# Performance work log

Hardware: AMD Instinct MI355X
Metric: run time of the kernel (lower is better)

## Reference

```python
import jax, jax.numpy as jnp
import numpy as np

MAXTIME = 1406073600
MINTIME = 832550400
SPAN = 10000
TIME_EMB = 100
N_GATE = 8
NUM_INTEREST = 4
DIM = 64
SEQ = 256
BATCH = 1024
ALPHA = 0.1
PI = 3.14159  # matches the literal in the source


def _build_time_table():
    # TimeEncoder: interleaved sin/cos positional table over time buckets.
    n = MAXTIME // SPAN + 3
    pos = np.arange(n, dtype=np.float64)[:, None]
    div = np.exp(np.arange(TIME_EMB // 2, dtype=np.float64) * -(np.log(10000.0) / TIME_EMB))[None, :]
    te = np.zeros((n, TIME_EMB), dtype=np.float32)
    te[:, 0::2] = np.sin(pos * div)
    te[:, 1::2] = np.cos(pos * div)
    return jnp.asarray(te)

_TIME_TABLE = _build_time_table()


def _time_encode(t):
    idx = (t / SPAN).astype(jnp.int32)
    return _TIME_TABLE[idx - jnp.min(idx)]


def setup_inputs() -> dict:
    key = jax.random.key(0)
    ks = jax.random.split(key, 11)
    B, S, D, NI, G = BATCH, SEQ, DIM, NUM_INTEREST, N_GATE
    item_his_emb = jax.random.normal(ks[0], (B, S, D), jnp.float32)
    item_eb = jax.random.normal(ks[1], (B, D), jnp.float32)
    # query times near maxtime, history times strictly earlier -> positive deltas
    t_batch = MAXTIME - 1e6 * jax.random.uniform(ks[2], (B,), jnp.float32)
    t_his = MINTIME + (MAXTIME - MINTIME - 1e6) * jax.random.uniform(ks[3], (B, S), jnp.float32)
    mask = (jax.random.uniform(ks[4], (B, S)) > 0.3).astype(jnp.float32)
    W1 = jax.random.normal(ks[5], (3 * TIME_EMB, 100), jnp.float32) / np.sqrt(3 * TIME_EMB)
    b1 = jnp.zeros((100,), jnp.float32)
    W2 = jax.random.normal(ks[6], (100, 1), jnp.float32) * 0.1
    b2 = jnp.zeros((1,), jnp.float32)
    phase = 100000.0 * jax.random.uniform(ks[7], (1, 1, G), jnp.float32)
    tao = 86400.0 * jnp.array([[[1, 2, 7, 14, 30, 60, 365, 730]]], jnp.float32)
    ratio = 0.3 * jax.random.uniform(ks[8], (1, 1, G), jnp.float32)
    gate_emb = jax.random.normal(ks[9], (1, D, G), jnp.float32)
    w_bilinear = jax.random.normal(ks[10], (S, NI * D, D), jnp.float32)
    return {"item_his_emb": item_his_emb, "item_eb": item_eb, "t_batch": t_batch,
            "t_his": t_his, "mask": mask, "W1": W1, "b1": b1, "W2": W2, "b2": b2,
            "phase": phase, "tao": tao, "ratio": ratio, "gate_emb": gate_emb,
            "w_bilinear": w_bilinear, "ta": 2}


def reference(item_his_emb, item_eb, t_batch, t_his, mask, W1, b1, W2, b2,
              phase, tao, ratio, gate_emb, w_bilinear, ta):
    B, S, D = item_his_emb.shape
    NI = NUM_INTEREST
    # --- time factor ---
    t_tiled = jnp.broadcast_to(t_batch[:, None], (B, S))
    time_feature = jnp.concatenate([_time_encode(t_tiled), _time_encode(t_his),
                                    _time_encode(t_tiled - t_his)], axis=2)  # [B,S,300]
    hidden1 = jax.nn.relu(time_feature @ W1 + b1)
    t_factor = jnp.transpose(jax.nn.sigmoid(hidden1 @ W2 + b2), (0, 2, 1))  # [B,1,S]
    # --- circadian gate factor ---
    phi = jnp.mod(t_his[:, :, None] - phase, tao) / tao  # [B,S,G]
    gate = jnp.where(phi < ratio, jnp.maximum(jnp.sin(PI * phi / ratio), 0.0), ALPHA * phi)
    gate_ratio = jax.nn.softmax(jnp.einsum('bsd,dg->bsg', item_his_emb, gate_emb[0]), axis=2) * gate
    g_factor = jnp.sum(gate_ratio, axis=2)[:, None, :]  # [B,1,S]
    reg1 = jnp.linalg.norm(t_factor)
    reg2 = jnp.linalg.norm(ratio) + jnp.linalg.norm(phase) / 100000.0
    # ta == 2 branch
    loss_reg = 0.1 * reg1 + 1.0 * reg2 + 1.0 / reg1 + 0.1 / reg2
    factor = jnp.broadcast_to(t_factor + g_factor, (B, NI, S))
    # --- bilinear_type == 2 projection ---
    item_emb_hat = jnp.einsum('skd,bsd->bsk', w_bilinear, item_his_emb)  # [B,S,NI*D]
    item_emb_hat = item_emb_hat.reshape(B, S, NI, D).transpose(0, 2, 1, 3)  # [B,NI,S,D]
    hat_iter = jax.lax.stop_gradient(item_emb_hat)
    # --- dynamic routing, 3 iterations ---
    cw = jnp.zeros((B, NI, S), item_his_emb.dtype)
    amask = mask[:, None, :]
    cap = None
    for i in range(3):
        sw = jax.nn.softmax(cw, axis=1)           # softmax over interests
        sw = jnp.where(amask == 0, 0.0, sw)
        src = hat_iter if i < 2 else item_emb_hat
        cap = jnp.einsum('bks,bksd->bkd', sw, src)  # [B,NI,D]
        n2 = jnp.sum(cap * cap, axis=-1, keepdims=True)
        cap = (n2 / (1.0 + n2) / jnp.sqrt(n2 + 1e-9)) * cap  # squash
        if i < 2:
            delta = jnp.einsum('bksd,bkd->bks', hat_iter, cap) * factor
            cw = cw + delta
    interest_capsule = cap  # [B,NI,D]
    # --- hard readout ---
    atten = jax.nn.softmax(jnp.einsum('bkd,bd->bk', interest_capsule, item_eb), axis=1)
    readout = interest_capsule[jnp.arange(B), jnp.argmax(atten, axis=1)]  # [B,D]
    return interest_capsule, readout, loss_reg
```

## Files before the change

kernel.cpp:

```cpp
#include <hip/hip_runtime.h>
#include <math.h>
#include <limits.h>

#define BB 1024
#define SS 256
#define DD 64
#define NI 4
#define NG 8
#define TE_N 100
#define PMAX 57420
#define PMAXP 57424
#define P0MAX 128
#define TPB2 64
#define NPAIR ((size_t)BB*SS)

typedef _Float16 half8 __attribute__((ext_vector_type(8)));
typedef _Float16 half4 __attribute__((ext_vector_type(4)));
typedef float f32x4 __attribute__((ext_vector_type(4)));

#define OFF_FTHT  ((size_t)0)
#define OFF_FDFT  ((size_t)TE_N*PMAXP)
#define OFF_GTBP  (OFF_FDFT + (size_t)TE_N*PMAXP)
#define OFF_FAC   (OFF_GTBP + (size_t)TE_N*P0MAX)
#define OFF_SCAL  (OFF_FAC + (size_t)BB*SS)
#define OFF_REC   (OFF_SCAL + 160)
#define OFF_SREC  (OFF_REC + NPAIR*2)
#define OFF_ZP    (OFF_SREC + NPAIR*2)
#define OFF_HAT   (OFF_ZP + 4*NPAIR)

__device__ inline float dpp_add_xor1(float x){
    int i = __builtin_bit_cast(int, x);
    int p = __builtin_amdgcn_update_dpp(i, i, 0xB1, 0xF, 0xF, true);
    return x + __builtin_bit_cast(float, p);
}
__device__ inline float dpp_add_xor2(float x){
    int i = __builtin_bit_cast(int, x);
    int p = __builtin_amdgcn_update_dpp(i, i, 0x4E, 0xF, 0xF, true);
    return x + __builtin_bit_cast(float, p);
}
__device__ inline float swz_add_xor16(float x){
    int i = __builtin_bit_cast(int, x);
    int p = __builtin_amdgcn_ds_swizzle(i, 0x401F);
    return x + __builtin_bit_cast(float, p);
}

__global__ void k_init(float* ws){
    int t = threadIdx.x;
    int* ib = (int*)(ws + OFF_SCAL);
    if (t == 0){
        ib[0] = INT_MAX; ib[1] = INT_MAX; ib[2] = INT_MAX;
        ws[OFF_SCAL + 4] = 0.0f;
    }
    if (t >= 8 && t < 136) ib[t] = 0;
}

__global__ void k_min(const float* __restrict__ tb, const float* __restrict__ th, float* ws){
    int gid = blockIdx.x * blockDim.x + threadIdx.x;
    int stride = gridDim.x * blockDim.x;
    int m0 = INT_MAX, m1 = INT_MAX, m2 = INT_MAX;
    for (int i = gid; i < BB*SS; i += stride){
        float t  = th[i];
        float t2 = tb[i >> 8];
        int i1 = (int)(t / 10000.0f);
        int i2 = (int)((t2 - t) / 10000.0f);
        m1 = min(m1, i1);
        m2 = min(m2, i2);
    }
    if (gid < BB) m0 = (int)(tb[gid] / 10000.0f);
    #pragma unroll
    for (int off = 1; off < 64; off <<= 1){
        m0 = min(m0, __shfl_xor(m0, off));
        m1 = min(m1, __shfl_xor(m1, off));
        m2 = min(m2, __shfl_xor(m2, off));
    }
    if ((threadIdx.x & 63) == 0){
        int* mi = (int*)(ws + OFF_SCAL);
        atomicMin(mi + 0, m0);
        atomicMin(mi + 1, m1);
        atomicMin(mi + 2, m2);
    }
}

__global__ void __launch_bounds__(256) k_tables(const float* __restrict__ W1, float* ws){
    int pbase = blockIdx.x * TPB2;
    int t = threadIdx.x;
    __shared__ float te[TPB2][102];
    for (int idx = t; idx < TPB2*50; idx += 256){
        int pp = idx / 50, h = idx - pp*50;
        double div = exp((double)h * -0.09210340371976184);
        double a = (double)(pbase + pp) * div;
        te[pp][2*h]   = (float)sin(a);
        te[pp][2*h+1] = (float)cos(a);
    }
    __syncthreads();
    #pragma unroll 5
    for (int k = 0; k < 25; k++){
        int o = t + 256*k;
        int j = __builtin_amdgcn_readfirstlane(o >> 6);
        int pp = o & 63;
        int p = pbase + pp;
        float a1 = 0.f, a2 = 0.f;
        for (int i = 0; i < TE_N; i++){
            float v = te[pp][i];
            a1 += v * W1[(100+i)*100 + j];
            a2 += v * W1[(200+i)*100 + j];
        }
        if (p < PMAX){
            ws[OFF_FTHT + (size_t)j*PMAXP + p] = a1;
            ws[OFF_FDFT + (size_t)j*PMAXP + p] = a2;
        }
    }
}

__global__ void k_gtbP(const float* __restrict__ W1, const float* __restrict__ b1, float* ws){
    int p0 = blockIdx.x;
    int t = threadIdx.x;
    __shared__ float te[TE_N];
    if (t < TE_N/2){
        double div = exp((double)t * -0.09210340371976184);
        double a = (double)p0 * div;
        te[2*t]   = (float)sin(a);
        te[2*t+1] = (float)cos(a);
    }
    __syncthreads();
    if (t < TE_N){
        float a1 = b1[t];
        for (int i = 0; i < TE_N; i++) a1 += te[i] * W1[i*100 + t];
        ws[OFF_GTBP + (size_t)t*P0MAX + p0] = a1;
    }
}

__global__ void __launch_bounds__(256) k_hist(const float* __restrict__ tb,
                                              const float* __restrict__ th, float* ws){
    __shared__ int lh[64];
    int t = threadIdx.x;
    if (t < 64) lh[t] = 0;
    __syncthreads();
    int gid = blockIdx.x*256 + t;
    int b = gid >> 8;
    const int* mi = (const int*)(ws + OFF_SCAL);
    float thv = th[gid], tbv = tb[b];
    int p1 = (int)(thv / 10000.0f) - mi[1];
    int p2 = (int)((tbv - thv) / 10000.0f) - mi[2];
    int p0 = (int)(tbv / 10000.0f) - mi[0];
    p1 = min(max(p1, 0), PMAX-1);
    p2 = min(max(p2, 0), PMAX-1);
    p0 = min(max(p0, 0), P0MAX-1);
    ((uint2*)(ws + OFF_REC))[gid] =
        make_uint2((unsigned)p1 | ((unsigned)p2 << 16), (unsigned)gid | ((unsigned)p0 << 20));
    atomicAdd(&lh[p1 >> 10], 1);
    __syncthreads();
    if (t < 64 && lh[t]) atomicAdd((int*)(ws + OFF_SCAL) + 8 + t, lh[t]);
}

__global__ void k_scan(float* ws){
    if (threadIdx.x == 0){
        int* g   = (int*)(ws + OFF_SCAL) + 8;
        int* cur = (int*)(ws + OFF_SCAL) + 72;
        int acc = 0;
        for (int i = 0; i < 64; i++){ cur[i] = acc; acc += g[i]; }
    }
}

__global__ void __launch_bounds__(256) k_scatter(float* ws){
    __shared__ int lh[64], lbase[64];
    int t = threadIdx.x;
    if (t < 64) lh[t] = 0;
    __syncthreads();
    int gid = blockIdx.x*256 + t;
    uint2 r = ((const uint2*)(ws + OFF_REC))[gid];
    int bkt = (int)(r.x & 0xFFFFu) >> 10;
    int myloc = atomicAdd(&lh[bkt], 1);
    __syncthreads();
    if (t < 64 && lh[t]) lbase[t] = atomicAdd((int*)(ws + OFF_SCAL) + 72 + t, lh[t]);
    __syncthreads();
    ((uint2*)(ws + OFF_SREC))[lbase[bkt] + myloc] = r;
}

__global__ void __launch_bounds__(256) k_factor2(const float* __restrict__ W2, float* ws){
    int t = threadIdx.x;
    int bid = blockIdx.x;
    int jh  = blockIdx.y;
    int sbid = (bid & 7)*128 + (bid >> 3);
    int q = sbid*256 + t;
    uint2 r = ((const uint2*)(ws + OFF_SREC))[q];
    int p1  = (int)(r.x & 0xFFFFu);
    int p2  = (int)(r.x >> 16);
    int p0  = (int)(r.y >> 20);

    const float* ft = ws + OFF_FTHT + (size_t)(jh*25)*PMAXP + p1;
    const float* fd = ws + OFF_FDFT + (size_t)(jh*25)*PMAXP + p2;
    const float* gp = ws + OFF_GTBP + (size_t)(jh*25)*P0MAX + p0;
    const float* w2 = W2 + jh*25;

    float z = 0.f;
    #pragma unroll
    for (int j = 0; j < 25; j++){
        float a = ft[(size_t)j*PMAXP];
        float c = fd[(size_t)j*PMAXP];
        float g = gp[(size_t)j*P0MAX];
        z += fmaxf(g + a + c, 0.f) * w2[j];
    }
    ws[OFF_ZP + (size_t)jh*NPAIR + q] = z;
}

__global__ void __launch_bounds__(256) k_fsig(const float* __restrict__ b2, float* ws){
    int q = blockIdx.x*256 + threadIdx.x;
    float z = (ws[OFF_ZP + q] + ws[OFF_ZP + NPAIR + q])
            + (ws[OFF_ZP + 2*NPAIR + q] + ws[OFF_ZP + 3*NPAIR + q]);
    unsigned ry = ((const uint2*)(ws + OFF_SREC))[q].y;
    int gid = (int)(ry & 0xFFFFFu);
    float tf = 1.f / (1.f + expf(-(z + b2[0])));
    ws[OFF_FAC + gid] = tf;
    float r1 = tf * tf;
    #pragma unroll
    for (int off = 1; off < 64; off <<= 1) r1 += __shfl_xor(r1, off);
    if ((threadIdx.x & 63) == 0) atomicAdd(ws + OFF_SCAL + 4, r1);
}

__global__ void __launch_bounds__(256) k_gate(const float* __restrict__ X,
      const float* __restrict__ th_, const float* __restrict__ phase,
      const float* __restrict__ tao, const float* __restrict__ ratio,
      const float* __restrict__ ge, float* ws){
    __shared__ float sge[NG][DD];
    int t = threadIdx.x;
    for (int i = t; i < DD*NG; i += 256) sge[i & 7][i >> 3] = ge[i];
    __syncthreads();
    int gid = blockIdx.x * 256 + t;

    float lg[NG];
    #pragma unroll
    for (int g = 0; g < NG; g++) lg[g] = 0.f;
    const float4* xr = (const float4*)(X + (size_t)gid*DD);
    #pragma unroll 4
    for (int dc = 0; dc < 16; dc++){
        float4 xv = xr[dc];
        #pragma unroll
        for (int g = 0; g < NG; g++){
            lg[g] += xv.x*sge[g][dc*4+0] + xv.y*sge[g][dc*4+1]
                   + xv.z*sge[g][dc*4+2] + xv.w*sge[g][dc*4+3];
        }
    }
    float mx = lg[0];
    #pragma unroll
    for (int g = 1; g < NG; g++) mx = fmaxf(mx, lg[g]);
    float thv = th_[gid];
    float es = 0.f, gf = 0.f;
    #pragma unroll
    for (int g = 0; g < NG; g++){
        float e = expf(lg[g] - mx);
        es += e;
        float phv = fmodf(thv - phase[g], tao[g]) / tao[g];
        float gv = (phv < ratio[g]) ? fmaxf(sinf(3.14159f*phv/ratio[g]), 0.f) : 0.1f*phv;
        gf += e * gv;
    }
    ws[OFF_FAC + gid] += gf / es;
}

__global__ void __launch_bounds__(512, 2)
k_hat(const float* __restrict__ X, const float* __restrict__ Wb,
      float* __restrict__ hat, int b0, int nb){
    int btile = blockIdx.x;
    int s     = blockIdx.y;
    int t     = threadIdx.x;
    int rows = nb - btile*64; if (rows > 64) rows = 64;

    __shared__ _Float16 lds[40960];

    const float* xbase = X + ((size_t)(b0 + btile*64)*SS + s)*DD;
    #pragma unroll
    for (int i = 0; i < 2; i++){
        int q = t + 512*i;
        int r = q >> 4, jf = q & 15;
        float4 v;
        if (r < rows) v = *(const float4*)(xbase + (size_t)r*SS*DD + jf*4);
        else { v.x = 0.f; v.y = 0.f; v.z = 0.f; v.w = 0.f; }
        half4 h, l;
        h.x = (_Float16)v.x; h.y = (_Float16)v.y; h.z = (_Float16)v.z; h.w = (_Float16)v.w;
        l.x = (_Float16)(v.x - (float)h.x); l.y = (_Float16)(v.y - (float)h.y);
        l.z = (_Float16)(v.z - (float)h.z); l.w = (_Float16)(v.w - (float)h.w);
        int bt = r >> 4, rowin = r & 15;
        int j0 = jf*4;
        int kk = j0 >> 5, jb = (j0 & 31) >> 3, e0 = j0 & 7;
        int lane = rowin + 16*jb;
        int base = ((bt*2 + kk)*2)*512 + lane*8 + e0;
        *(half4*)(lds + base)       = h;
        *(half4*)(lds + base + 512) = l;
    }
    const float* wbase = Wb + (size_t)s*16384;
    #pragma unroll
    for (int i = 0; i < 8; i++){
        int q = t + 512*i;
        int kd = q >> 4, jf = q & 15;
        float4 v = *(const float4*)(wbase + kd*64 + jf*4);
        half4 h, l;
        h.x = (_Float16)v.x; h.y = (_Float16)v.y; h.z = (_Float16)v.z; h.w = (_Float16)v.w;
        l.x = (_Float16)(v.x - (float)h.x); l.y = (_Float16)(v.y - (float)h.y);
        l.z = (_Float16)(v.z - (float)h.z); l.w = (_Float16)(v.w - (float)h.w);
        int kdt = kd >> 4, rowin = kd & 15;
        int j0 = jf*4;
        int kk = j0 >> 5, jb = (j0 & 31) >> 3, e0 = j0 & 7;
        int lane = rowin + 16*jb;
        int base = 8192 + ((kdt*2 + kk)*2)*512 + lane*8 + e0;
        *(half4*)(lds + base)       = h;
        *(half4*)(lds + base + 512) = l;
    }
    __syncthreads();

    int w    = t >> 6;
    int lane = t & 63;
    int wbt  = w >> 1;
    int kdh  = w & 1;

    half8 a[2][2];
    #pragma unroll
    for (int kk = 0; kk < 2; kk++)
        #pragma unroll
        for (int hl = 0; hl < 2; hl++)
            a[kk][hl] = *(half8*)(lds + ((wbt*2 + kk)*2 + hl)*512 + lane*8);

    int brow = (lane >> 4) * 4;
    int bcol = lane & 15;

    #pragma unroll
    for (int kdti = 0; kdti < 8; kdti++){
        int kdt = kdh*8 + kdti;
        const _Float16* wb0 = lds + 8192 + ((kdt*2 + 0)*2)*512 + lane*8;
        const _Float16* wb1 = lds + 8192 + ((kdt*2 + 1)*2)*512 + lane*8;
        half8 bh0 = *(half8*)(wb0);
        half8 bl0 = *(half8*)(wb0 + 512);
        half8 bh1 = *(half8*)(wb1);
        half8 bl1 = *(half8*)(wb1 + 512);
        f32x4 acc = {0.f, 0.f, 0.f, 0.f};
        acc = __builtin_amdgcn_mfma_f32_16x16x32_f16(a[0][0], bh0, acc, 0, 0, 0);
        acc = __builtin_amdgcn_mfma_f32_16x16x32_f16(a[0][0], bl0, acc, 0, 0, 0);
        acc = __builtin_amdgcn_mfma_f32_16x16x32_f16(a[0][1], bh0, acc, 0, 0, 0);
        acc = __builtin_amdgcn_mfma_f32_16x16x32_f16(a[1][0], bh1, acc, 0, 0, 0);
        acc = __builtin_amdgcn_mfma_f32_16x16x32_f16(a[1][0], bl1, acc, 0, 0, 0);
        acc = __builtin_amdgcn_mfma_f32_16x16x32_f16(a[1][1], bh1, acc, 0, 0, 0);
        int kd = kdt*16 + bcol;
        #pragma unroll
        for (int r = 0; r < 4; r++){
            int rl = wbt*16 + brow + r;
            if (rl < rows)
                hat[((size_t)(btile*64 + rl)*SS + s)*256 + kd] = acc[r];
        }
    }
}

__global__ void __launch_bounds__(1024) k_route(const float* __restrict__ eb,
                                                const float* __restrict__ mask_,
                                                const float* __restrict__ ws,
                                                const float* __restrict__ hat,
                                                float* __restrict__ out, int b0){
    int bl = blockIdx.x;
    int b = b0 + bl;
    int t = threadIdx.x;
    int lane = t & 63, wv = t >> 6;
    int k = (lane >> 2) & 3;
    int s_local = (lane & 3) | (((lane >> 4) & 3) << 2);
    int s = wv * 16 + s_local;
    __shared__ float part[16][4][64];
    __shared__ float capl[4][68];
    __shared__ float logits[4];
    __shared__ int kms;

    float hat_r[64];
    const float4* hsrc = (const float4*)(hat + (size_t)bl*65536 + ((size_t)s*4 + k)*64);
    #pragma unroll
    for (int jc = 0; jc < 16; jc++){
        float4 v = hsrc[jc];
        hat_r[4*jc] = v.x; hat_r[4*jc+1] = v.y; hat_r[4*jc+2] = v.z; hat_r[4*jc+3] = v.w;
    }
    float fac = ws[OFF_FAC + (size_t)b*SS + s];
    float mk = mask_[(size_t)b*SS + s];
    float cw = 0.f;
    float capv = 0.f;

    for (int it = 0; it < 3; ++it){
        float sw;
        if (it == 0){
            sw = (mk == 0.f) ? 0.f : 0.25f;
        } else {
            float m = fmaxf(cw, __shfl_xor(cw, 4)); m = fmaxf(m, __shfl_xor(m, 8));
            float e = expf(cw - m);
            float ssum = e + __shfl_xor(e, 4); ssum += __shfl_xor(ssum, 8);
            sw = (mk == 0.f) ? 0.f : (e / ssum);
        }

        #pragma unroll
        for (int c = 0; c < 4; c++){
            float tmp[16];
            #pragma unroll
            for (int i = 0; i < 16; i++) tmp[i] = sw * hat_r[c*16 + i];
            #pragma unroll
            for (int i = 0; i < 16; i++) tmp[i] = dpp_add_xor1(tmp[i]);
            #pragma unroll
            for (int i = 0; i < 16; i++) tmp[i] = dpp_add_xor2(tmp[i]);
            #pragma unroll
            for (int i = 0; i < 16; i++) tmp[i] = swz_add_xor16(tmp[i]);
            #pragma unroll
            for (int i = 0; i < 16; i++) tmp[i] += __shfl_xor(tmp[i], 32);
            if ((lane & 0x33) == 0){
                float* dst = &part[wv][lane >> 2][c*16];
                #pragma unroll
                for (int i = 0; i < 4; i++)
                    ((float4*)dst)[i] = make_float4(tmp[4*i], tmp[4*i+1], tmp[4*i+2], tmp[4*i+3]);
            }
        }
        __syncthreads();
        if (t < 256){
            int k2 = t >> 6, d = t & 63;
            float cp = 0.f;
            #pragma unroll
            for (int w2 = 0; w2 < 16; w2++) cp += part[w2][k2][d];
            float q = cp * cp;
            #pragma unroll
            for (int msk = 1; msk < 64; msk <<= 1) q += __shfl_xor(q, msk);
            float sc = q / ((1.f + q) * sqrtf(q + 1e-9f));
            capv = sc * cp;
            capl[k2][d] = capv;
        }
        __syncthreads();
        if (it < 2){
            const float4* cp4 = (const float4*)&capl[k][0];
            float dot = 0.f;
            #pragma unroll
            for (int jc = 0; jc < 16; jc++){
                float4 v = cp4[jc];
                dot += hat_r[4*jc]*v.x + hat_r[4*jc+1]*v.y + hat_r[4*jc+2]*v.z + hat_r[4*jc+3]*v.w;
            }
            cw += dot * fac;
        }
        __syncthreads();
    }

    if (t < 256){
        int k2 = t >> 6, d = t & 63;
        out[(size_t)b*256 + t] = capv;
        float qq = capv * eb[(size_t)b*DD + d];
        #pragma unroll
        for (int msk = 1; msk < 64; msk <<= 1) qq += __shfl_xor(qq, msk);
        if (lane == 0) logits[k2] = qq;
    }
    __syncthreads();
    if (t == 0){
        float best = logits[0]; int km = 0;
        for (int kk = 1; kk < 4; kk++) if (logits[kk] > best){ best = logits[kk]; km = kk; }
        kms = km;
    }
    __syncthreads();
    if (t < 64) out[(size_t)BB*256 + (size_t)b*64 + t] = capl[kms][t];
}

__global__ void k_final(const float* __restrict__ phase, const float* __restrict__ ratio,
                        float* ws, float* __restrict__ out){
    if (threadIdx.x == 0){
        float r2a = 0.f, r2b = 0.f;
        for (int g = 0; g < NG; g++){ r2a += ratio[g]*ratio[g]; r2b += phase[g]*phase[g]; }
        float reg2 = sqrtf(r2a) + sqrtf(r2b) / 100000.0f;
        float reg1 = sqrtf(ws[OFF_SCAL + 4]);
        out[(size_t)BB*256 + (size_t)BB*64] = 0.1f*reg1 + reg2 + 1.0f/reg1 + 0.1f/reg2;
    }
}

extern "C" void kernel_launch(void* const* d_in, const int* in_sizes, int n_in,
                              void* d_out, int out_size, void* d_ws, size_t ws_size,
                              hipStream_t stream){
    const float* Xh = (const float*)d_in[0];
    const float* eb = (const float*)d_in[1];
    const float* tb = (const float*)d_in[2];
    const float* th = (const float*)d_in[3];
    const float* mk = (const float*)d_in[4];
    const float* W1 = (const float*)d_in[5];
    const float* b1 = (const float*)d_in[6];
    const float* W2 = (const float*)d_in[7];
    const float* b2 = (const float*)d_in[8];
    const float* ph = (const float*)d_in[9];
    const float* ta = (const float*)d_in[10];
    const float* ra = (const float*)d_in[11];
    const float* ge = (const float*)d_in[12];
    const float* wb = (const float*)d_in[13];
    float* out = (float*)d_out;
    float* ws  = (float*)d_ws;

    hipLaunchKernelGGL(k_init,    dim3(1),     dim3(256), 0, stream, ws);
    hipLaunchKernelGGL(k_min,     dim3(256),   dim3(256), 0, stream, tb, th, ws);
    hipLaunchKernelGGL(k_tables,  dim3((PMAX+TPB2-1)/TPB2), dim3(256), 0, stream, W1, ws);
    hipLaunchKernelGGL(k_gtbP,    dim3(P0MAX), dim3(128), 0, stream, W1, b1, ws);
    hipLaunchKernelGGL(k_hist,    dim3(BB),    dim3(256), 0, stream, tb, th, ws);
    hipLaunchKernelGGL(k_scan,    dim3(1),     dim3(64),  0, stream, ws);
    hipLaunchKernelGGL(k_scatter, dim3(BB),    dim3(256), 0, stream, ws);
    hipLaunchKernelGGL(k_factor2, dim3(1024, 4), dim3(256), 0, stream, W2, ws);
    hipLaunchKernelGGL(k_fsig,    dim3(1024),  dim3(256), 0, stream, b2, ws);
    hipLaunchKernelGGL(k_gate,    dim3(BB),    dim3(256), 0, stream, Xh, th, ph, ta, ra, ge, ws);

    long wfloats  = (long)(ws_size / sizeof(float));
    long hatavail = wfloats - (long)OFF_HAT;
    int CH = (int)(hatavail / 65536);
    if (CH > BB) CH = BB;
    if (CH >= 128) CH &= ~127;
    if (CH < 1)  CH = 1;
    float* hatbuf = ws + OFF_HAT;
    for (int c0 = 0; c0 < BB; c0 += CH){
        int nb = BB - c0; if (nb > CH) nb = CH;
        int nbt = (nb + 63) / 64;
        hipLaunchKernelGGL(k_hat,   dim3(nbt, 256), dim3(512),  0, stream, Xh, wb, hatbuf, c0, nb);
        hipLaunchKernelGGL(k_route, dim3(nb),       dim3(1024), 0, stream, eb, mk, ws, hatbuf, out, c0);
    }
    hipLaunchKernelGGL(k_final, dim3(1), dim3(64), 0, stream, ph, ra, ws, out);
}
```

Baseline: 608.7 us.

## Register-tile time-table projection per output column and stage results through LDS

The table-building kernel now gives each thread one output column and has it accumulate over 16 table positions in registers. Each W1 weight is therefore loaded once per 16 positions instead of once per position. Results are transposed through shared memory so the global stores stay coalesced along the position axis. The cost is more blocks with smaller 128-thread groups, 28 of the 128 threads idle during the compute phase, and higher register use.

```diff
diff --git a/kernel.cpp b/kernel.cpp
--- a/kernel.cpp
+++ b/kernel.cpp
@@ -11,7 +11,7 @@
 #define PMAX 57420
 #define PMAXP 57424
 #define P0MAX 128
-#define TPB2 64
+#define TPB 16
 #define NPAIR ((size_t)BB*SS)
 
 typedef _Float16 half8 __attribute__((ext_vector_type(8)));
@@ -81,11 +81,13 @@
     }
 }
 
-__global__ void __launch_bounds__(256) k_tables(const float* __restrict__ W1, float* ws){
-    int pbase = blockIdx.x * TPB2;
-    int t = threadIdx.x;
-    __shared__ float te[TPB2][102];
-    for (int idx = t; idx < TPB2*50; idx += 256){
+__global__ void __launch_bounds__(128) k_tables(const float* __restrict__ W1, float* ws){
+    int pbase = blockIdx.x * TPB;
+    int t = threadIdx.x;
+    __shared__ float te[TPB][TE_N];
+    __shared__ float tr1[TPB][104];
+    __shared__ float tr2[TPB][104];
+    for (int idx = t; idx < TPB*50; idx += 128){
         int pp = idx / 50, h = idx - pp*50;
         double div = exp((double)h * -0.09210340371976184);
         double a = (double)(pbase + pp) * div;
@@ -93,21 +95,33 @@
         te[pp][2*h+1] = (float)cos(a);
     }
     __syncthreads();
-    #pragma unroll 5
-    for (int k = 0; k < 25; k++){
-        int o = t + 256*k;
-        int j = __builtin_amdgcn_readfirstlane(o >> 6);
-        int pp = o & 63;
+    if (t < TE_N){
+        float a1[TPB], a2[TPB];
+        #pragma unroll
+        for (int pp = 0; pp < TPB; pp++){ a1[pp] = 0.f; a2[pp] = 0.f; }
+        for (int i = 0; i < TE_N; i++){
+            float w1v = W1[(100+i)*100 + t];
+            float w2v = W1[(200+i)*100 + t];
+            #pragma unroll
+            for (int pp = 0; pp < TPB; pp++){
+                float v = te[pp][i];
+                a1[pp] += v * w1v;
+                a2[pp] += v * w2v;
+            }
+        }
+        #pragma unroll
+        for (int pp = 0; pp < TPB; pp++){
+            tr1[pp][t] = a1[pp];
+            tr2[pp][t] = a2[pp];
+        }
+    }
+    __syncthreads();
+    for (int idx = t; idx < TPB*TE_N; idx += 128){
+        int j = idx >> 4, pp = idx & 15;
         int p = pbase + pp;
-        float a1 = 0.f, a2 = 0.f;
-        for (int i = 0; i < TE_N; i++){
-            float v = te[pp][i];
-            a1 += v * W1[(100+i)*100 + j];
-            a2 += v * W1[(200+i)*100 + j];
-        }
         if (p < PMAX){
-            ws[OFF_FTHT + (size_t)j*PMAXP + p] = a1;
-            ws[OFF_FDFT + (size_t)j*PMAXP + p] = a2;
+            ws[OFF_FTHT + (size_t)j*PMAXP + p] = tr1[pp][j];
+            ws[OFF_FDFT + (size_t)j*PMAXP + p] = tr2[pp][j];
         }
     }
 }
@@ -486,7 +500,7 @@
 
     hipLaunchKernelGGL(k_init,    dim3(1),     dim3(256), 0, stream, ws);
     hipLaunchKernelGGL(k_min,     dim3(256),   dim3(256), 0, stream, tb, th, ws);
-    hipLaunchKernelGGL(k_tables,  dim3((PMAX+TPB2-1)/TPB2), dim3(256), 0, stream, W1, ws);
+    hipLaunchKernelGGL(k_tables,  dim3((PMAX+TPB-1)/TPB), dim3(128), 0, stream, W1, ws);
     hipLaunchKernelGGL(k_gtbP,    dim3(P0MAX), dim3(128), 0, stream, W1, b1, ws);
     hipLaunchKernelGGL(k_hist,    dim3(BB),    dim3(256), 0, stream, tb, th, ws);
     hipLaunchKernelGGL(k_scan,    dim3(1),     dim3(64),  0, stream, ws);
```

New measurement: 544.3 us. 10.6% less time.
